# Optimization experiments

Hardware: AMD Instinct MI355X
Metric: run time of the kernel (lower is better)

The kernel has to match this reference:

```python
import jax, jax.numpy as jnp
import numpy as np

T, H, W = 4, 16, 16
S = T * H * W          # 1024 flattened sequence length
C = 576                # embd_dim
NH = 8                 # n_head
DK = C // NH           # 72 per-head dim
L = 4                  # n_layer
B = 4                  # batch
PD = C // 3            # 192 per-axis pos-embed dim


def setup_inputs() -> dict:
    key = jax.random.key(0)
    ks = jax.random.split(key, 10)
    s = 1.0 / np.sqrt(C)
    return {
        "x": jax.random.normal(ks[0], (B, T, H, W, C), jnp.float32),
        "pos0": jax.random.normal(ks[1], (T, PD), jnp.float32) * 0.01,
        "pos1": jax.random.normal(ks[2], (H, PD), jnp.float32) * 0.01,
        "pos2": jax.random.normal(ks[3], (W, PD), jnp.float32) * 0.01,
        "ln1_g": jnp.ones((L, C), jnp.float32),
        "ln1_b": jnp.zeros((L, C), jnp.float32),
        "wq": jax.random.normal(ks[4], (L, C, C), jnp.float32) * s,
        "wk": jax.random.normal(ks[5], (L, C, C), jnp.float32) * s,
        "wv": jax.random.normal(ks[6], (L, C, C), jnp.float32) * s,
        "wo": jax.random.normal(ks[7], (L, C, C), jnp.float32) * (s / np.sqrt(L)),
        "wo_b": jnp.zeros((L, C), jnp.float32),
        "ln2_g": jnp.ones((L, C), jnp.float32),
        "ln2_b": jnp.zeros((L, C), jnp.float32),
        "w1": jax.random.normal(ks[8], (L, C, 4 * C), jnp.float32) * s,
        "b1": jnp.zeros((L, 4 * C), jnp.float32),
        "w2": jax.random.normal(ks[9], (L, 4 * C, C), jnp.float32) * (s / 2.0),
        "b2": jnp.zeros((L, C), jnp.float32),
    }


def _layernorm(x, g, b):
    # Faithful to the source: float32 math, and (1e-5 + rsqrt(var)) multiplier
    # (note: source adds eps to rsqrt, not to var -- replicated exactly).
    xf = x.astype(jnp.float32)
    mu = xf.mean(-1, keepdims=True)
    var = jnp.mean(jnp.square(xf - mu), -1, keepdims=True)
    y = (xf - mu) * (1e-5 + jax.lax.rsqrt(var)) * g + b
    return y.astype(x.dtype)


def _stack(x, pos0, pos1, pos2, ln1_g, ln1_b, wq, wk, wv, wo, wo_b,
           ln2_g, ln2_b, w1, b1, w2, b2):
    b = x.shape[0]
    xf = x.reshape(b, S, C)
    # right_shift (decode_step=None): shift flattened tokens right by one
    xf = jnp.pad(xf[:, :-1], ((0, 0), (1, 0), (0, 0)))
    # broadcast positional embedding, concat along channel
    pos = jnp.concatenate([
        jnp.broadcast_to(pos0[:, None, None, :], (T, H, W, PD)),
        jnp.broadcast_to(pos1[None, :, None, :], (T, H, W, PD)),
        jnp.broadcast_to(pos2[None, None, :, :], (T, H, W, PD)),
    ], axis=-1).reshape(S, C)
    xf = xf + pos

    causal = jnp.tril(jnp.ones((S, S), bool))
    scale = 1.0 / np.sqrt(DK)
    neg_inf = jnp.float32(-jnp.inf)

    for l in range(L):  # fixed small layer loop
        # --- causal full self-attention ---
        h = _layernorm(xf, ln1_g[l], ln1_b[l])
        q = (h @ wq[l]).reshape(b, S, NH, DK).transpose(0, 2, 1, 3)
        k = (h @ wk[l]).reshape(b, S, NH, DK).transpose(0, 2, 1, 3)
        v = (h @ wv[l]).reshape(b, S, NH, DK).transpose(0, 2, 1, 3)
        att = jnp.einsum('bhqd,bhkd->bhqk', q, k) * scale
        att = jnp.where(causal, att, neg_inf)
        att = jax.nn.softmax(att, axis=-1)
        a = jnp.einsum('bhqk,bhkd->bhqd', att, v)
        a = a.transpose(0, 2, 1, 3).reshape(b, S, C)
        xf = xf + a @ wo[l] + wo_b[l]
        # --- FFN with GeLU2: sigmoid(1.702*x)*x ---
        h = _layernorm(xf, ln2_g[l], ln2_b[l])
        h = h @ w1[l] + b1[l]
        h = jax.nn.sigmoid(1.702 * h) * h
        xf = xf + h @ w2[l] + b2[l]
    return xf.reshape(b, T, H, W, C)


def reference(x, pos0, pos1, pos2, ln1_g, ln1_b, wq, wk, wv, wo, wo_b,
              ln2_g, ln2_b, w1, b1, w2, b2):
    return _stack(x, pos0, pos1, pos2, ln1_g, ln1_b, wq, wk, wv, wo, wo_b,
                  ln2_g, ln2_b, w1, b1, w2, b2)
```

## Files before the change

kernel.cpp:

```cpp
#include <hip/hip_runtime.h>
#include <hip/hip_bf16.h>

typedef __hip_bfloat16 bf16;
using bf16x8 = __attribute__((ext_vector_type(8))) short;
using f32x4  = __attribute__((ext_vector_type(4))) float;

#define S_LEN 1024
#define CDIM  576
#define NHEAD 8
#define DKH   72
#define BATCH 4
#define MROWS 4096
#define FFDIM 2304

__global__ __launch_bounds__(256) void transpose_cvt(
    const float* __restrict__ in, bf16* __restrict__ out, int K, int N) {
  __shared__ float tile[32][33];
  const size_t mat = (size_t)K * N;
  const float* inl = in + (size_t)blockIdx.z * mat;
  bf16* outl = out + (size_t)blockIdx.z * mat;
  int n0 = blockIdx.x * 32, k0 = blockIdx.y * 32;
  int tx = threadIdx.x & 31, ty = threadIdx.x >> 5;
#pragma unroll
  for (int i = 0; i < 32; i += 8)
    tile[ty + i][tx] = inl[(size_t)(k0 + ty + i) * N + (n0 + tx)];
  __syncthreads();
#pragma unroll
  for (int i = 0; i < 32; i += 8)
    outl[(size_t)(n0 + ty + i) * K + (k0 + tx)] = __float2bfloat16(tile[tx][ty + i]);
}

__global__ __launch_bounds__(256) void build_xf(
    const float* __restrict__ x, const float* __restrict__ p0,
    const float* __restrict__ p1, const float* __restrict__ p2,
    float* __restrict__ xf) {
  int idx = blockIdx.x * 256 + threadIdx.x;
  int c4 = idx % 144;
  int s  = (idx / 144) & (S_LEN - 1);
  int b  = idx / (144 * S_LEN);
  int c  = c4 * 4;
  int t = s >> 8, hh = (s >> 4) & 15, w = s & 15;
  float4 pv;
  if (c < 192)       pv = *(const float4*)&p0[t  * 192 + c];
  else if (c < 384)  pv = *(const float4*)&p1[hh * 192 + c - 192];
  else               pv = *(const float4*)&p2[w  * 192 + c - 384];
  float4 xv = make_float4(0.f, 0.f, 0.f, 0.f);
  if (s > 0) xv = *(const float4*)&x[((size_t)b * S_LEN + s - 1) * CDIM + c];
  float4 r = make_float4(xv.x + pv.x, xv.y + pv.y, xv.z + pv.z, xv.w + pv.w);
  *(float4*)&xf[((size_t)b * S_LEN + s) * CDIM + c] = r;
}

__global__ __launch_bounds__(256) void ln_kernel(
    const float* __restrict__ x, const float* __restrict__ g,
    const float* __restrict__ b, bf16* __restrict__ out) {
  int row  = blockIdx.x * 4 + (threadIdx.x >> 6);
  int lane = threadIdx.x & 63;
  const float* xr = x + (size_t)row * CDIM;
  float vals[9];
  float sum = 0.f;
#pragma unroll
  for (int i = 0; i < 9; i++) { vals[i] = xr[lane + 64 * i]; sum += vals[i]; }
#pragma unroll
  for (int o = 1; o < 64; o <<= 1) sum += __shfl_xor(sum, o);
  float mu = sum * (1.f / CDIM);
  float vs = 0.f;
#pragma unroll
  for (int i = 0; i < 9; i++) { float d = vals[i] - mu; vs += d * d; }
#pragma unroll
  for (int o = 1; o < 64; o <<= 1) vs += __shfl_xor(vs, o);
  float mult = 1e-5f + rsqrtf(vs * (1.f / CDIM));
  bf16* orow = out + (size_t)row * CDIM;
#pragma unroll
  for (int i = 0; i < 9; i++) {
    int c = lane + 64 * i;
    orow[c] = __float2bfloat16((vals[i] - mu) * mult * g[c] + b[c]);
  }
}

template <bool BIAS, bool RES, int ACT, bool OUTBF>
__global__ __launch_bounds__(256) void gemm_kernel(
    const bf16* __restrict__ A, const bf16* __restrict__ Bt,
    const float* __restrict__ bias, const float* __restrict__ res,
    void* __restrict__ outp, int M, int N, int K) {
  __shared__ short ldsA[64][40];
  __shared__ short ldsB[64][40];
  int m0 = blockIdx.x * 64, n0 = blockIdx.y * 64;
  int tid = threadIdx.x;
  int wave = tid >> 6, lane = tid & 63;
  int wm = (wave & 1) * 32, wn = (wave >> 1) * 32;
  int lrow = lane & 15, lq = lane >> 4;
  f32x4 acc[2][2] = {};
  int srow = tid >> 2, skc = (tid & 3) * 8;
  const short* Ag = ((const short*)A) + (size_t)(m0 + srow) * K + skc;
  const short* Bg = ((const short*)Bt) + (size_t)(n0 + srow) * K + skc;
  for (int k0 = 0; k0 < K; k0 += 32) {
    *(bf16x8*)&ldsA[srow][skc] = *(const bf16x8*)(Ag + k0);
    *(bf16x8*)&ldsB[srow][skc] = *(const bf16x8*)(Bg + k0);
    __syncthreads();
    bf16x8 af[2], bfv[2];
#pragma unroll
    for (int mi = 0; mi < 2; mi++) af[mi]  = *(const bf16x8*)&ldsA[wm + mi * 16 + lrow][lq * 8];
#pragma unroll
    for (int ni = 0; ni < 2; ni++) bfv[ni] = *(const bf16x8*)&ldsB[wn + ni * 16 + lrow][lq * 8];
#pragma unroll
    for (int mi = 0; mi < 2; mi++)
#pragma unroll
      for (int ni = 0; ni < 2; ni++)
        acc[mi][ni] = __builtin_amdgcn_mfma_f32_16x16x32_bf16(af[mi], bfv[ni], acc[mi][ni], 0, 0, 0);
    __syncthreads();
  }
#pragma unroll
  for (int mi = 0; mi < 2; mi++)
#pragma unroll
    for (int ni = 0; ni < 2; ni++) {
      int col = n0 + wn + ni * 16 + lrow;
#pragma unroll
      for (int r = 0; r < 4; r++) {
        int rowi = m0 + wm + mi * 16 + lq * 4 + r;
        float v = acc[mi][ni][r];
        if (BIAS) v += bias[col];
        if (ACT == 1) v = v / (1.f + __expf(-1.702f * v));
        size_t idx = (size_t)rowi * N + col;
        if (RES) v += res[idx];
        if (OUTBF) ((bf16*)outp)[idx] = __float2bfloat16(v);
        else       ((float*)outp)[idx] = v;
      }
    }
}

__device__ __forceinline__ short f2bf_bits(float x) {
  unsigned int u = __float_as_uint(x);
  u += 0x7fffu + ((u >> 16) & 1u);
  return (short)(u >> 16);
}

__global__ __launch_bounds__(256) void attn_mfma(
    const bf16* __restrict__ q, const bf16* __restrict__ k,
    const bf16* __restrict__ v, bf16* __restrict__ a) {
  __shared__ short ldsK[64][104];
  __shared__ short ldsVt[96][72];
  __shared__ short ldsP[4][16][72];
  int bh = blockIdx.y;
  int b = bh >> 3, h = bh & 7;
  int tid = threadIdx.x, wave = tid >> 6, lane = tid & 63;
  int lr = lane & 15, quad = lane >> 4;
  const float scale = 0.11785113019775793f;

  for (int half = 0; half < 2; half++) {
    int qt = half == 0 ? blockIdx.x : 15 - blockIdx.x;
    int qrow = qt * 64 + wave * 16 + lr;
    const short* qg = ((const short*)q) + ((size_t)(b * S_LEN + qrow)) * CDIM + h * DKH;
    bf16x8 qfrag[3];
#pragma unroll
    for (int c = 0; c < 3; c++) {
      int d0 = c * 32 + quad * 8;
      bf16x8 z = {0, 0, 0, 0, 0, 0, 0, 0};
      qfrag[c] = (d0 < DKH) ? *(const bf16x8*)(qg + d0) : z;
    }
    f32x4 oacc[6] = {};
    float m[4], l[4];
#pragma unroll
    for (int r = 0; r < 4; r++) { m[r] = -1e30f; l[r] = 0.f; }

    for (int kt = 0; kt <= qt; kt++) {
      __syncthreads();
      {
        int key = tid & 63;
        int dgb = tid >> 6;
        const short* kgr = ((const short*)k) + ((size_t)(b * S_LEN + kt * 64 + key)) * CDIM + h * DKH;
        const short* vgr = ((const short*)v) + ((size_t)(b * S_LEN + kt * 64 + key)) * CDIM + h * DKH;
#pragma unroll
        for (int pass = 0; pass < 3; pass++) {
          int d0 = (dgb + pass * 4) * 8;
          bf16x8 kv = {0, 0, 0, 0, 0, 0, 0, 0};
          bf16x8 vv = {0, 0, 0, 0, 0, 0, 0, 0};
          if (d0 < DKH) { kv = *(const bf16x8*)(kgr + d0); vv = *(const bf16x8*)(vgr + d0); }
          *(bf16x8*)&ldsK[key][d0] = kv;
#pragma unroll
          for (int j = 0; j < 8; j++) ldsVt[d0 + j][key] = vv[j];
        }
      }
      __syncthreads();
      f32x4 sacc[4] = {};
#pragma unroll
      for (int nc = 0; nc < 4; nc++)
#pragma unroll
        for (int c = 0; c < 3; c++) {
          bf16x8 kf = *(const bf16x8*)&ldsK[nc * 16 + lr][c * 32 + quad * 8];
          sacc[nc] = __builtin_amdgcn_mfma_f32_16x16x32_bf16(qfrag[c], kf, sacc[nc], 0, 0, 0);
        }
      float tmax[4];
#pragma unroll
      for (int r = 0; r < 4; r++) tmax[r] = -1e30f;
      bool diag = (kt == qt);
#pragma unroll
      for (int nc = 0; nc < 4; nc++)
#pragma unroll
        for (int r = 0; r < 4; r++) {
          float s = sacc[nc][r] * scale;
          if (diag && (nc * 16 + lr > wave * 16 + quad * 4 + r)) s = -1e30f;
          sacc[nc][r] = s;
          tmax[r] = fmaxf(tmax[r], s);
        }
#pragma unroll
      for (int r = 0; r < 4; r++) {
        tmax[r] = fmaxf(tmax[r], __shfl_xor(tmax[r], 1));
        tmax[r] = fmaxf(tmax[r], __shfl_xor(tmax[r], 2));
        tmax[r] = fmaxf(tmax[r], __shfl_xor(tmax[r], 4));
        tmax[r] = fmaxf(tmax[r], __shfl_xor(tmax[r], 8));
      }
      float alpha[4], psum[4];
#pragma unroll
      for (int r = 0; r < 4; r++) {
        float mn = fmaxf(m[r], tmax[r]);
        alpha[r] = __expf(m[r] - mn);
        m[r] = mn;
        psum[r] = 0.f;
      }
#pragma unroll
      for (int nc = 0; nc < 4; nc++)
#pragma unroll
        for (int r = 0; r < 4; r++) {
          float p = __expf(sacc[nc][r] - m[r]);
          psum[r] += p;
          ldsP[wave][quad * 4 + r][nc * 16 + lr] = f2bf_bits(p);
        }
#pragma unroll
      for (int r = 0; r < 4; r++) {
        psum[r] += __shfl_xor(psum[r], 1);
        psum[r] += __shfl_xor(psum[r], 2);
        psum[r] += __shfl_xor(psum[r], 4);
        psum[r] += __shfl_xor(psum[r], 8);
        l[r] = l[r] * alpha[r] + psum[r];
      }
#pragma unroll
      for (int dc = 0; dc < 6; dc++)
#pragma unroll
        for (int r = 0; r < 4; r++) oacc[dc][r] *= alpha[r];
      __builtin_amdgcn_sched_barrier(0);
      bf16x8 pfrag[2];
#pragma unroll
      for (int kc = 0; kc < 2; kc++)
        pfrag[kc] = *(const bf16x8*)&ldsP[wave][lr][kc * 32 + quad * 8];
#pragma unroll
      for (int dc = 0; dc < 6; dc++)
#pragma unroll
        for (int kc = 0; kc < 2; kc++) {
          bf16x8 vf = *(const bf16x8*)&ldsVt[dc * 16 + lr][kc * 32 + quad * 8];
          oacc[dc] = __builtin_amdgcn_mfma_f32_16x16x32_bf16(pfrag[kc], vf, oacc[dc], 0, 0, 0);
        }
    }

#pragma unroll
    for (int dc = 0; dc < 6; dc++) {
      int d = dc * 16 + lr;
      if (d < DKH) {
#pragma unroll
        for (int r = 0; r < 4; r++) {
          int row = qt * 64 + wave * 16 + quad * 4 + r;
          float val = oacc[dc][r] / l[r];
          a[((size_t)(b * S_LEN + row)) * CDIM + h * DKH + d] = __float2bfloat16(val);
        }
      }
    }
  }
}

extern "C" void kernel_launch(void* const* d_in, const int* in_sizes, int n_in,
                              void* d_out, int out_size, void* d_ws, size_t ws_size,
                              hipStream_t stream) {
  const float* x    = (const float*)d_in[0];
  const float* pos0 = (const float*)d_in[1];
  const float* pos1 = (const float*)d_in[2];
  const float* pos2 = (const float*)d_in[3];
  const float* ln1g = (const float*)d_in[4];
  const float* ln1b = (const float*)d_in[5];
  const float* wq   = (const float*)d_in[6];
  const float* wk   = (const float*)d_in[7];
  const float* wv   = (const float*)d_in[8];
  const float* wo   = (const float*)d_in[9];
  const float* wob  = (const float*)d_in[10];
  const float* ln2g = (const float*)d_in[11];
  const float* ln2b = (const float*)d_in[12];
  const float* w1   = (const float*)d_in[13];
  const float* b1   = (const float*)d_in[14];
  const float* w2   = (const float*)d_in[15];
  const float* b2   = (const float*)d_in[16];

  char* ws = (char*)d_ws;
  size_t off = 0;
  auto alloc = [&](size_t bytes) {
    char* p = ws + off;
    off += (bytes + 255) & ~(size_t)255;
    return p;
  };
  const size_t wsz  = (size_t)4 * CDIM * CDIM * sizeof(bf16);
  const size_t wsz2 = (size_t)4 * CDIM * FFDIM * sizeof(bf16);
  bf16* wqT = (bf16*)alloc(wsz);
  bf16* wkT = (bf16*)alloc(wsz);
  bf16* wvT = (bf16*)alloc(wsz);
  bf16* woT = (bf16*)alloc(wsz);
  bf16* w1T = (bf16*)alloc(wsz2);
  bf16* w2T = (bf16*)alloc(wsz2);
  bf16* hbuf = (bf16*)alloc((size_t)MROWS * CDIM * sizeof(bf16));
  bf16* abuf = (bf16*)alloc((size_t)MROWS * CDIM * sizeof(bf16));
  bf16* ubuf = (bf16*)alloc((size_t)MROWS * FFDIM * sizeof(bf16));
  bf16* qb   = (bf16*)alloc((size_t)MROWS * CDIM * sizeof(bf16));
  bf16* kb   = (bf16*)alloc((size_t)MROWS * CDIM * sizeof(bf16));
  bf16* vb   = (bf16*)alloc((size_t)MROWS * CDIM * sizeof(bf16));
  float* xf  = (float*)d_out;

  transpose_cvt<<<dim3(18, 18, 4), 256, 0, stream>>>(wq, wqT, CDIM, CDIM);
  transpose_cvt<<<dim3(18, 18, 4), 256, 0, stream>>>(wk, wkT, CDIM, CDIM);
  transpose_cvt<<<dim3(18, 18, 4), 256, 0, stream>>>(wv, wvT, CDIM, CDIM);
  transpose_cvt<<<dim3(18, 18, 4), 256, 0, stream>>>(wo, woT, CDIM, CDIM);
  transpose_cvt<<<dim3(72, 18, 4), 256, 0, stream>>>(w1, w1T, CDIM, FFDIM);
  transpose_cvt<<<dim3(18, 72, 4), 256, 0, stream>>>(w2, w2T, FFDIM, CDIM);

  build_xf<<<2304, 256, 0, stream>>>(x, pos0, pos1, pos2, xf);

  for (int l = 0; l < 4; l++) {
    const size_t wo_off = (size_t)l * CDIM * CDIM;
    const size_t w1_off = (size_t)l * CDIM * FFDIM;
    ln_kernel<<<1024, 256, 0, stream>>>(xf, ln1g + l * CDIM, ln1b + l * CDIM, hbuf);
    gemm_kernel<false, false, 0, true><<<dim3(64, 9), 256, 0, stream>>>(
        hbuf, wqT + wo_off, nullptr, nullptr, qb, MROWS, CDIM, CDIM);
    gemm_kernel<false, false, 0, true><<<dim3(64, 9), 256, 0, stream>>>(
        hbuf, wkT + wo_off, nullptr, nullptr, kb, MROWS, CDIM, CDIM);
    gemm_kernel<false, false, 0, true><<<dim3(64, 9), 256, 0, stream>>>(
        hbuf, wvT + wo_off, nullptr, nullptr, vb, MROWS, CDIM, CDIM);
    attn_mfma<<<dim3(8, 32), 256, 0, stream>>>(qb, kb, vb, abuf);
    gemm_kernel<true, true, 0, false><<<dim3(64, 9), 256, 0, stream>>>(
        abuf, woT + wo_off, wob + l * CDIM, xf, xf, MROWS, CDIM, CDIM);
    ln_kernel<<<1024, 256, 0, stream>>>(xf, ln2g + l * CDIM, ln2b + l * CDIM, hbuf);
    gemm_kernel<true, false, 1, true><<<dim3(64, 36), 256, 0, stream>>>(
        hbuf, w1T + w1_off, b1 + l * FFDIM, nullptr, ubuf, MROWS, FFDIM, CDIM);
    gemm_kernel<true, true, 0, false><<<dim3(64, 9), 256, 0, stream>>>(
        ubuf, w2T + w1_off, b2 + l * CDIM, xf, xf, MROWS, CDIM, FFDIM);
  }
}
```

Before: 814.8 us.

## Fuse QKV projection, add LDS-direct-load GEMM with BK=64, split attention blocks

Concatenates the Q, K and V weights into one padded transposed matrix so a single GEMM writes a packed QKV buffer, and attention reads from it. The GEMM is rewritten to load tiles with global_load_lds into a fragment-ordered LDS layout, uses a K step of 64 and offers a 128-wide N tile. Attention now gives each block a single query tile instead of pairing two, loads K via direct-to-LDS, and trims the V/O padding from 96 to 80 dims. Output weights are zero-padded to 640 columns with memsets, which adds setup work, and 128-wide tiles reduce the block count.

```diff
diff --git a/kernel.cpp b/kernel.cpp
--- a/kernel.cpp
+++ b/kernel.cpp
@@ -12,13 +12,28 @@
 #define BATCH 4
 #define MROWS 4096
 #define FFDIM 2304
+#define QKVN  1728
+#define QKVNP 1792
+#define CPAD  640
+
+__device__ __forceinline__ void gload16(const void* g, void* l) {
+  __builtin_amdgcn_global_load_lds(
+      (const __attribute__((address_space(1))) unsigned int*)g,
+      (__attribute__((address_space(3))) unsigned int*)l, 16, 0, 0);
+}
+
+__device__ __forceinline__ short f2bf_bits(float x) {
+  unsigned int u = __float_as_uint(x);
+  u += 0x7fffu + ((u >> 16) & 1u);
+  return (short)(u >> 16);
+}
 
 __global__ __launch_bounds__(256) void transpose_cvt(
-    const float* __restrict__ in, bf16* __restrict__ out, int K, int N) {
+    const float* __restrict__ in, bf16* __restrict__ out, int K, int N,
+    size_t in_ls, size_t out_ls) {
   __shared__ float tile[32][33];
-  const size_t mat = (size_t)K * N;
-  const float* inl = in + (size_t)blockIdx.z * mat;
-  bf16* outl = out + (size_t)blockIdx.z * mat;
+  const float* inl = in + (size_t)blockIdx.z * in_ls;
+  bf16* outl = out + (size_t)blockIdx.z * out_ls;
   int n0 = blockIdx.x * 32, k0 = blockIdx.y * 32;
   int tx = threadIdx.x & 31, ty = threadIdx.x >> 5;
 #pragma unroll
@@ -77,190 +92,204 @@
   }
 }
 
-template <bool BIAS, bool RES, int ACT, bool OUTBF>
-__global__ __launch_bounds__(256) void gemm_kernel(
+template <int BN, bool BIAS, bool RES, int ACT, bool OUTBF>
+__global__ __launch_bounds__(256) void gemm2(
     const bf16* __restrict__ A, const bf16* __restrict__ Bt,
     const float* __restrict__ bias, const float* __restrict__ res,
-    void* __restrict__ outp, int M, int N, int K) {
-  __shared__ short ldsA[64][40];
-  __shared__ short ldsB[64][40];
-  int m0 = blockIdx.x * 64, n0 = blockIdx.y * 64;
-  int tid = threadIdx.x;
-  int wave = tid >> 6, lane = tid & 63;
-  int wm = (wave & 1) * 32, wn = (wave >> 1) * 32;
-  int lrow = lane & 15, lq = lane >> 4;
-  f32x4 acc[2][2] = {};
-  int srow = tid >> 2, skc = (tid & 3) * 8;
-  const short* Ag = ((const short*)A) + (size_t)(m0 + srow) * K + skc;
-  const short* Bg = ((const short*)Bt) + (size_t)(n0 + srow) * K + skc;
-  for (int k0 = 0; k0 < K; k0 += 32) {
-    *(bf16x8*)&ldsA[srow][skc] = *(const bf16x8*)(Ag + k0);
-    *(bf16x8*)&ldsB[srow][skc] = *(const bf16x8*)(Bg + k0);
+    void* __restrict__ outp, int Nreal, int ostride, int K) {
+  constexpr int NI = BN / 32;
+  constexpr int BSTR = BN / 16;
+  __shared__ short ldsA[2 * 4 * 512];
+  __shared__ short ldsB[2 * BSTR * 512];
+  const int tid = threadIdx.x, lane = tid & 63, wave = tid >> 6;
+  const int lr = lane & 15, quad = lane >> 4;
+  const int m0 = blockIdx.x * 64, n0 = blockIdx.y * BN;
+  const int wm = (wave & 1) * 32, wn = (wave >> 1) * (BN / 2);
+  f32x4 acc[2][NI] = {};
+  const short* Ag  = (const short*)A  + (size_t)(m0 + wave * 16 + lr) * K + quad * 8;
+  const short* Bg0 = (const short*)Bt + (size_t)(n0 + wave * 16 + lr) * K + quad * 8;
+  const short* Bg1 = (const short*)Bt + (size_t)(n0 + (wave + 4) * 16 + lr) * K + quad * 8;
+
+  for (int k0 = 0; k0 < K; k0 += 64) {
     __syncthreads();
-    bf16x8 af[2], bfv[2];
-#pragma unroll
-    for (int mi = 0; mi < 2; mi++) af[mi]  = *(const bf16x8*)&ldsA[wm + mi * 16 + lrow][lq * 8];
-#pragma unroll
-    for (int ni = 0; ni < 2; ni++) bfv[ni] = *(const bf16x8*)&ldsB[wn + ni * 16 + lrow][lq * 8];
-#pragma unroll
-    for (int mi = 0; mi < 2; mi++)
-#pragma unroll
-      for (int ni = 0; ni < 2; ni++)
-        acc[mi][ni] = __builtin_amdgcn_mfma_f32_16x16x32_bf16(af[mi], bfv[ni], acc[mi][ni], 0, 0, 0);
+#pragma unroll
+    for (int kc = 0; kc < 2; kc++) {
+      gload16(Ag + k0 + kc * 32, &ldsA[(kc * 4 + wave) * 512]);
+      gload16(Bg0 + k0 + kc * 32, &ldsB[(kc * BSTR + wave) * 512]);
+      if (BN == 128) gload16(Bg1 + k0 + kc * 32, &ldsB[(kc * BSTR + wave + 4) * 512]);
+    }
     __syncthreads();
-  }
+#pragma unroll
+    for (int kc = 0; kc < 2; kc++) {
+      bf16x8 af[2], bfv[NI];
+#pragma unroll
+      for (int mi = 0; mi < 2; mi++)
+        af[mi] = *(const bf16x8*)&ldsA[(kc * 4 + (wave & 1) * 2 + mi) * 512 + lane * 8];
+#pragma unroll
+      for (int ni = 0; ni < NI; ni++)
+        bfv[ni] = *(const bf16x8*)&ldsB[(kc * BSTR + (wave >> 1) * NI + ni) * 512 + lane * 8];
+#pragma unroll
+      for (int mi = 0; mi < 2; mi++)
+#pragma unroll
+        for (int ni = 0; ni < NI; ni++)
+          acc[mi][ni] = __builtin_amdgcn_mfma_f32_16x16x32_bf16(af[mi], bfv[ni], acc[mi][ni], 0, 0, 0);
+    }
+  }
+
+  float* fout = (float*)outp;
+  bf16*  bout = (bf16*)outp;
 #pragma unroll
   for (int mi = 0; mi < 2; mi++)
 #pragma unroll
-    for (int ni = 0; ni < 2; ni++) {
-      int col = n0 + wn + ni * 16 + lrow;
-#pragma unroll
-      for (int r = 0; r < 4; r++) {
-        int rowi = m0 + wm + mi * 16 + lq * 4 + r;
-        float v = acc[mi][ni][r];
-        if (BIAS) v += bias[col];
-        if (ACT == 1) v = v / (1.f + __expf(-1.702f * v));
-        size_t idx = (size_t)rowi * N + col;
-        if (RES) v += res[idx];
-        if (OUTBF) ((bf16*)outp)[idx] = __float2bfloat16(v);
-        else       ((float*)outp)[idx] = v;
-      }
-    }
-}
-
-__device__ __forceinline__ short f2bf_bits(float x) {
-  unsigned int u = __float_as_uint(x);
-  u += 0x7fffu + ((u >> 16) & 1u);
-  return (short)(u >> 16);
+    for (int ni = 0; ni < NI; ni++) {
+      int col = n0 + wn + ni * 16 + lr;
+      if (col < Nreal) {
+#pragma unroll
+        for (int r = 0; r < 4; r++) {
+          int row = m0 + wm + mi * 16 + quad * 4 + r;
+          float v = acc[mi][ni][r];
+          if (BIAS) v += bias[col];
+          if (ACT == 1) v = v / (1.f + __expf(-1.702f * v));
+          size_t idx = (size_t)row * ostride + col;
+          if (RES) v += res[idx];
+          if (OUTBF) bout[idx] = __float2bfloat16(v);
+          else       fout[idx] = v;
+        }
+      }
+    }
 }
 
 __global__ __launch_bounds__(256) void attn_mfma(
-    const bf16* __restrict__ q, const bf16* __restrict__ k,
-    const bf16* __restrict__ v, bf16* __restrict__ a) {
-  __shared__ short ldsK[64][104];
-  __shared__ short ldsVt[96][72];
-  __shared__ short ldsP[4][16][72];
-  int bh = blockIdx.y;
-  int b = bh >> 3, h = bh & 7;
-  int tid = threadIdx.x, wave = tid >> 6, lane = tid & 63;
-  int lr = lane & 15, quad = lane >> 4;
+    const bf16* __restrict__ qkv, bf16* __restrict__ a) {
+  __shared__ short ldsK[12 * 512];
+  __shared__ short ldsVt[80][104];
+  __shared__ short ldsP[4 * 1024];
+  const int bh = blockIdx.y, b = bh >> 3, h = bh & 7;
+  const int tid = threadIdx.x, wave = tid >> 6, lane = tid & 63;
+  const int lr = lane & 15, quad = lane >> 4;
+  const int qt = 15 - (int)blockIdx.x;
   const float scale = 0.11785113019775793f;
-
-  for (int half = 0; half < 2; half++) {
-    int qt = half == 0 ? blockIdx.x : 15 - blockIdx.x;
-    int qrow = qt * 64 + wave * 16 + lr;
-    const short* qg = ((const short*)q) + ((size_t)(b * S_LEN + qrow)) * CDIM + h * DKH;
-    bf16x8 qfrag[3];
-#pragma unroll
-    for (int c = 0; c < 3; c++) {
-      int d0 = c * 32 + quad * 8;
-      bf16x8 z = {0, 0, 0, 0, 0, 0, 0, 0};
-      qfrag[c] = (d0 < DKH) ? *(const bf16x8*)(qg + d0) : z;
-    }
-    f32x4 oacc[6] = {};
-    float m[4], l[4];
-#pragma unroll
-    for (int r = 0; r < 4; r++) { m[r] = -1e30f; l[r] = 0.f; }
-
-    for (int kt = 0; kt <= qt; kt++) {
-      __syncthreads();
-      {
-        int key = tid & 63;
-        int dgb = tid >> 6;
-        const short* kgr = ((const short*)k) + ((size_t)(b * S_LEN + kt * 64 + key)) * CDIM + h * DKH;
-        const short* vgr = ((const short*)v) + ((size_t)(b * S_LEN + kt * 64 + key)) * CDIM + h * DKH;
-#pragma unroll
-        for (int pass = 0; pass < 3; pass++) {
-          int d0 = (dgb + pass * 4) * 8;
-          bf16x8 kv = {0, 0, 0, 0, 0, 0, 0, 0};
+  const int qcol = h * DKH, kcol = CDIM + h * DKH, vcol = 2 * CDIM + h * DKH;
+
+  const int qrow = qt * 64 + wave * 16 + lr;
+  const short* qg = (const short*)qkv + (size_t)(b * S_LEN + qrow) * QKVN + qcol;
+  bf16x8 qfrag[3];
+#pragma unroll
+  for (int c = 0; c < 3; c++) {
+    int d0 = c * 32 + quad * 8;
+    bf16x8 z = {0, 0, 0, 0, 0, 0, 0, 0};
+    qfrag[c] = (d0 < DKH) ? *(const bf16x8*)(qg + d0) : z;
+  }
+  f32x4 oacc[5] = {};
+  float m[4], l[4];
+#pragma unroll
+  for (int r = 0; r < 4; r++) { m[r] = -1e30f; l[r] = 0.f; }
+
+  for (int kt = 0; kt <= qt; kt++) {
+    __syncthreads();
+    {
+      const short* kg = (const short*)qkv +
+          (size_t)(b * S_LEN + kt * 64 + wave * 16 + lr) * QKVN + kcol + quad * 8;
+#pragma unroll
+      for (int c = 0; c < 3; c++)
+        gload16(kg + c * 32, &ldsK[(wave * 3 + c) * 512]);
+    }
+    {
+      int key = tid & 63, dgb = tid >> 6;
+      const short* vg = (const short*)qkv + (size_t)(b * S_LEN + kt * 64 + key) * QKVN + vcol;
+#pragma unroll
+      for (int pass = 0; pass < 3; pass++) {
+        int d0 = (dgb + pass * 4) * 8;
+        if (d0 < 80) {
           bf16x8 vv = {0, 0, 0, 0, 0, 0, 0, 0};
-          if (d0 < DKH) { kv = *(const bf16x8*)(kgr + d0); vv = *(const bf16x8*)(vgr + d0); }
-          *(bf16x8*)&ldsK[key][d0] = kv;
+          if (d0 < DKH) vv = *(const bf16x8*)(vg + d0);
 #pragma unroll
           for (int j = 0; j < 8; j++) ldsVt[d0 + j][key] = vv[j];
         }
       }
-      __syncthreads();
-      f32x4 sacc[4] = {};
-#pragma unroll
-      for (int nc = 0; nc < 4; nc++)
-#pragma unroll
-        for (int c = 0; c < 3; c++) {
-          bf16x8 kf = *(const bf16x8*)&ldsK[nc * 16 + lr][c * 32 + quad * 8];
-          sacc[nc] = __builtin_amdgcn_mfma_f32_16x16x32_bf16(qfrag[c], kf, sacc[nc], 0, 0, 0);
-        }
-      float tmax[4];
-#pragma unroll
-      for (int r = 0; r < 4; r++) tmax[r] = -1e30f;
-      bool diag = (kt == qt);
-#pragma unroll
-      for (int nc = 0; nc < 4; nc++)
-#pragma unroll
-        for (int r = 0; r < 4; r++) {
-          float s = sacc[nc][r] * scale;
-          if (diag && (nc * 16 + lr > wave * 16 + quad * 4 + r)) s = -1e30f;
-          sacc[nc][r] = s;
-          tmax[r] = fmaxf(tmax[r], s);
-        }
+    }
+    __syncthreads();
+    f32x4 sacc[4] = {};
+#pragma unroll
+    for (int nc = 0; nc < 4; nc++)
+#pragma unroll
+      for (int c = 0; c < 3; c++) {
+        bf16x8 kf = *(const bf16x8*)&ldsK[(nc * 3 + c) * 512 + lane * 8];
+        sacc[nc] = __builtin_amdgcn_mfma_f32_16x16x32_bf16(qfrag[c], kf, sacc[nc], 0, 0, 0);
+      }
+    float tmax[4];
+#pragma unroll
+    for (int r = 0; r < 4; r++) tmax[r] = -1e30f;
+    bool diag = (kt == qt);
+#pragma unroll
+    for (int nc = 0; nc < 4; nc++)
 #pragma unroll
       for (int r = 0; r < 4; r++) {
-        tmax[r] = fmaxf(tmax[r], __shfl_xor(tmax[r], 1));
-        tmax[r] = fmaxf(tmax[r], __shfl_xor(tmax[r], 2));
-        tmax[r] = fmaxf(tmax[r], __shfl_xor(tmax[r], 4));
-        tmax[r] = fmaxf(tmax[r], __shfl_xor(tmax[r], 8));
-      }
-      float alpha[4], psum[4];
+        float s = sacc[nc][r] * scale;
+        if (diag && (nc * 16 + lr > wave * 16 + quad * 4 + r)) s = -1e30f;
+        sacc[nc][r] = s;
+        tmax[r] = fmaxf(tmax[r], s);
+      }
+#pragma unroll
+    for (int r = 0; r < 4; r++) {
+      tmax[r] = fmaxf(tmax[r], __shfl_xor(tmax[r], 1));
+      tmax[r] = fmaxf(tmax[r], __shfl_xor(tmax[r], 2));
+      tmax[r] = fmaxf(tmax[r], __shfl_xor(tmax[r], 4));
+      tmax[r] = fmaxf(tmax[r], __shfl_xor(tmax[r], 8));
+    }
+    float alpha[4], psum[4];
+#pragma unroll
+    for (int r = 0; r < 4; r++) {
+      float mn = fmaxf(m[r], tmax[r]);
+      alpha[r] = __expf(m[r] - mn);
+      m[r] = mn;
+      psum[r] = 0.f;
+    }
+#pragma unroll
+    for (int nc = 0; nc < 4; nc++)
 #pragma unroll
       for (int r = 0; r < 4; r++) {
-        float mn = fmaxf(m[r], tmax[r]);
-        alpha[r] = __expf(m[r] - mn);
-        m[r] = mn;
-        psum[r] = 0.f;
-      }
-#pragma unroll
-      for (int nc = 0; nc < 4; nc++)
-#pragma unroll
-        for (int r = 0; r < 4; r++) {
-          float p = __expf(sacc[nc][r] - m[r]);
-          psum[r] += p;
-          ldsP[wave][quad * 4 + r][nc * 16 + lr] = f2bf_bits(p);
-        }
+        float p = __expf(sacc[nc][r] - m[r]);
+        psum[r] += p;
+        int col = nc * 16 + lr;
+        ldsP[wave * 1024 + (col >> 5) * 512 +
+             (((col >> 3) & 3) * 16 + quad * 4 + r) * 8 + (col & 7)] = f2bf_bits(p);
+      }
+#pragma unroll
+    for (int r = 0; r < 4; r++) {
+      psum[r] += __shfl_xor(psum[r], 1);
+      psum[r] += __shfl_xor(psum[r], 2);
+      psum[r] += __shfl_xor(psum[r], 4);
+      psum[r] += __shfl_xor(psum[r], 8);
+      l[r] = l[r] * alpha[r] + psum[r];
+    }
+#pragma unroll
+    for (int dc = 0; dc < 5; dc++)
+#pragma unroll
+      for (int r = 0; r < 4; r++) oacc[dc][r] *= alpha[r];
+    __builtin_amdgcn_sched_barrier(0);
+    bf16x8 pfrag[2];
+#pragma unroll
+    for (int kc = 0; kc < 2; kc++)
+      pfrag[kc] = *(const bf16x8*)&ldsP[wave * 1024 + kc * 512 + lane * 8];
+#pragma unroll
+    for (int dc = 0; dc < 5; dc++)
+#pragma unroll
+      for (int kc = 0; kc < 2; kc++) {
+        bf16x8 vf = *(const bf16x8*)&ldsVt[dc * 16 + lr][kc * 32 + quad * 8];
+        oacc[dc] = __builtin_amdgcn_mfma_f32_16x16x32_bf16(pfrag[kc], vf, oacc[dc], 0, 0, 0);
+      }
+  }
+
+#pragma unroll
+  for (int dc = 0; dc < 5; dc++) {
+    int d = dc * 16 + lr;
+    if (d < DKH) {
 #pragma unroll
       for (int r = 0; r < 4; r++) {
-        psum[r] += __shfl_xor(psum[r], 1);
-        psum[r] += __shfl_xor(psum[r], 2);
-        psum[r] += __shfl_xor(psum[r], 4);
-        psum[r] += __shfl_xor(psum[r], 8);
-        l[r] = l[r] * alpha[r] + psum[r];
-      }
-#pragma unroll
-      for (int dc = 0; dc < 6; dc++)
-#pragma unroll
-        for (int r = 0; r < 4; r++) oacc[dc][r] *= alpha[r];
-      __builtin_amdgcn_sched_barrier(0);
-      bf16x8 pfrag[2];
-#pragma unroll
-      for (int kc = 0; kc < 2; kc++)
-        pfrag[kc] = *(const bf16x8*)&ldsP[wave][lr][kc * 32 + quad * 8];
-#pragma unroll
-      for (int dc = 0; dc < 6; dc++)
-#pragma unroll
-        for (int kc = 0; kc < 2; kc++) {
-          bf16x8 vf = *(const bf16x8*)&ldsVt[dc * 16 + lr][kc * 32 + quad * 8];
-          oacc[dc] = __builtin_amdgcn_mfma_f32_16x16x32_bf16(pfrag[kc], vf, oacc[dc], 0, 0, 0);
-        }
-    }
-
-#pragma unroll
-    for (int dc = 0; dc < 6; dc++) {
-      int d = dc * 16 + lr;
-      if (d < DKH) {
-#pragma unroll
-        for (int r = 0; r < 4; r++) {
-          int row = qt * 64 + wave * 16 + quad * 4 + r;
-          float val = oacc[dc][r] / l[r];
-          a[((size_t)(b * S_LEN + row)) * CDIM + h * DKH + d] = __float2bfloat16(val);
-        }
+        int row = qt * 64 + wave * 16 + quad * 4 + r;
+        float val = oacc[dc][r] / l[r];
+        a[(size_t)(b * S_LEN + row) * CDIM + h * DKH + d] = __float2bfloat16(val);
       }
     }
   }
@@ -294,48 +323,57 @@
     off += (bytes + 255) & ~(size_t)255;
     return p;
   };
-  const size_t wsz  = (size_t)4 * CDIM * CDIM * sizeof(bf16);
-  const size_t wsz2 = (size_t)4 * CDIM * FFDIM * sizeof(bf16);
-  bf16* wqT = (bf16*)alloc(wsz);
-  bf16* wkT = (bf16*)alloc(wsz);
-  bf16* wvT = (bf16*)alloc(wsz);
-  bf16* woT = (bf16*)alloc(wsz);
-  bf16* w1T = (bf16*)alloc(wsz2);
-  bf16* w2T = (bf16*)alloc(wsz2);
-  bf16* hbuf = (bf16*)alloc((size_t)MROWS * CDIM * sizeof(bf16));
-  bf16* abuf = (bf16*)alloc((size_t)MROWS * CDIM * sizeof(bf16));
-  bf16* ubuf = (bf16*)alloc((size_t)MROWS * FFDIM * sizeof(bf16));
-  bf16* qb   = (bf16*)alloc((size_t)MROWS * CDIM * sizeof(bf16));
-  bf16* kb   = (bf16*)alloc((size_t)MROWS * CDIM * sizeof(bf16));
-  bf16* vb   = (bf16*)alloc((size_t)MROWS * CDIM * sizeof(bf16));
-  float* xf  = (float*)d_out;
-
-  transpose_cvt<<<dim3(18, 18, 4), 256, 0, stream>>>(wq, wqT, CDIM, CDIM);
-  transpose_cvt<<<dim3(18, 18, 4), 256, 0, stream>>>(wk, wkT, CDIM, CDIM);
-  transpose_cvt<<<dim3(18, 18, 4), 256, 0, stream>>>(wv, wvT, CDIM, CDIM);
-  transpose_cvt<<<dim3(18, 18, 4), 256, 0, stream>>>(wo, woT, CDIM, CDIM);
-  transpose_cvt<<<dim3(72, 18, 4), 256, 0, stream>>>(w1, w1T, CDIM, FFDIM);
-  transpose_cvt<<<dim3(18, 72, 4), 256, 0, stream>>>(w2, w2T, FFDIM, CDIM);
+  const size_t sz_qkvT = (size_t)4 * QKVNP * CDIM * sizeof(bf16);
+  const size_t sz_woT  = (size_t)4 * CPAD * CDIM * sizeof(bf16);
+  const size_t sz_w1T  = (size_t)4 * FFDIM * CDIM * sizeof(bf16);
+  const size_t sz_w2T  = (size_t)4 * CPAD * FFDIM * sizeof(bf16);
+  bf16* wqkvT = (bf16*)alloc(sz_qkvT);
+  bf16* woT   = (bf16*)alloc(sz_woT);
+  bf16* w1T   = (bf16*)alloc(sz_w1T);
+  bf16* w2T   = (bf16*)alloc(sz_w2T);
+  bf16* hbuf  = (bf16*)alloc((size_t)MROWS * CDIM * sizeof(bf16));
+  bf16* abuf  = (bf16*)alloc((size_t)MROWS * CDIM * sizeof(bf16));
+  bf16* ubuf  = (bf16*)alloc((size_t)MROWS * FFDIM * sizeof(bf16));
+  bf16* qkvb  = (bf16*)alloc((size_t)MROWS * QKVN * sizeof(bf16));
+  float* xf   = (float*)d_out;
+
+  hipMemsetAsync(wqkvT, 0, sz_qkvT, stream);
+  hipMemsetAsync(woT, 0, sz_woT, stream);
+  hipMemsetAsync(w2T, 0, sz_w2T, stream);
+
+  const size_t ils  = (size_t)CDIM * CDIM;
+  const size_t ils2 = (size_t)CDIM * FFDIM;
+  transpose_cvt<<<dim3(18, 18, 4), 256, 0, stream>>>(wq, wqkvT, CDIM, CDIM,
+      ils, (size_t)QKVNP * CDIM);
+  transpose_cvt<<<dim3(18, 18, 4), 256, 0, stream>>>(wk, wqkvT + (size_t)CDIM * CDIM, CDIM, CDIM,
+      ils, (size_t)QKVNP * CDIM);
+  transpose_cvt<<<dim3(18, 18, 4), 256, 0, stream>>>(wv, wqkvT + (size_t)2 * CDIM * CDIM, CDIM, CDIM,
+      ils, (size_t)QKVNP * CDIM);
+  transpose_cvt<<<dim3(18, 18, 4), 256, 0, stream>>>(wo, woT, CDIM, CDIM,
+      ils, (size_t)CPAD * CDIM);
+  transpose_cvt<<<dim3(72, 18, 4), 256, 0, stream>>>(w1, w1T, CDIM, FFDIM,
+      ils2, (size_t)FFDIM * CDIM);
+  transpose_cvt<<<dim3(18, 72, 4), 256, 0, stream>>>(w2, w2T, FFDIM, CDIM,
+      ils2, (size_t)CPAD * FFDIM);
 
   build_xf<<<2304, 256, 0, stream>>>(x, pos0, pos1, pos2, xf);
 
   for (int l = 0; l < 4; l++) {
-    const size_t wo_off = (size_t)l * CDIM * CDIM;
-    const size_t w1_off = (size_t)l * CDIM * FFDIM;
+    bf16* wqkv_l = wqkvT + (size_t)l * QKVNP * CDIM;
+    bf16* wo_l   = woT   + (size_t)l * CPAD * CDIM;
+    bf16* w1_l   = w1T   + (size_t)l * FFDIM * CDIM;
+    bf16* w2_l   = w2T   + (size_t)l * CPAD * FFDIM;
+
     ln_kernel<<<1024, 256, 0, stream>>>(xf, ln1g + l * CDIM, ln1b + l * CDIM, hbuf);
-    gemm_kernel<false, false, 0, true><<<dim3(64, 9), 256, 0, stream>>>(
-        hbuf, wqT + wo_off, nullptr, nullptr, qb, MROWS, CDIM, CDIM);
-    gemm_kernel<false, false, 0, true><<<dim3(64, 9), 256, 0, stream>>>(
-        hbuf, wkT + wo_off, nullptr, nullptr, kb, MROWS, CDIM, CDIM);
-    gemm_kernel<false, false, 0, true><<<dim3(64, 9), 256, 0, stream>>>(
-        hbuf, wvT + wo_off, nullptr, nullptr, vb, MROWS, CDIM, CDIM);
-    attn_mfma<<<dim3(8, 32), 256, 0, stream>>>(qb, kb, vb, abuf);
-    gemm_kernel<true, true, 0, false><<<dim3(64, 9), 256, 0, stream>>>(
-        abuf, woT + wo_off, wob + l * CDIM, xf, xf, MROWS, CDIM, CDIM);
+    gemm2<128, false, false, 0, true><<<dim3(64, QKVNP / 128), 256, 0, stream>>>(
+        hbuf, wqkv_l, nullptr, nullptr, qkvb, QKVN, QKVN, CDIM);
+    attn_mfma<<<dim3(16, 32), 256, 0, stream>>>(qkvb, abuf);
+    gemm2<64, true, true, 0, false><<<dim3(64, CPAD / 64), 256, 0, stream>>>(
+        abuf, wo_l, wob + l * CDIM, xf, xf, CDIM, CDIM, CDIM);
     ln_kernel<<<1024, 256, 0, stream>>>(xf, ln2g + l * CDIM, ln2b + l * CDIM, hbuf);
-    gemm_kernel<true, false, 1, true><<<dim3(64, 36), 256, 0, stream>>>(
-        hbuf, w1T + w1_off, b1 + l * FFDIM, nullptr, ubuf, MROWS, FFDIM, CDIM);
-    gemm_kernel<true, true, 0, false><<<dim3(64, 9), 256, 0, stream>>>(
-        ubuf, w2T + w1_off, b2 + l * CDIM, xf, xf, MROWS, CDIM, FFDIM);
-  }
-}
+    gemm2<128, true, false, 1, true><<<dim3(64, FFDIM / 128), 256, 0, stream>>>(
+        hbuf, w1_l, b1 + l * FFDIM, nullptr, ubuf, FFDIM, FFDIM, CDIM);
+    gemm2<64, true, true, 0, false><<<dim3(64, CPAD / 64), 256, 0, stream>>>(
+        ubuf, w2_l, b2 + l * CDIM, xf, xf, CDIM, CDIM, FFDIM);
+  }
+}
```

Result: slower. 950.5 us (+16.7%).
